# Optimization experiments

Measured on AMD Instinct MI355X. Metric: run time of the kernel, lower is better.

The kernel has to match this reference:

```python
import jax, jax.numpy as jnp
import numpy as np

B, S, DM = 2, 4096, 3584      # batch, seq_len, d_model (Zamba2-7B defaults)
H, DH = 112, 64               # n_heads, head_dim -> inner_dim = 7168
CHUNK = 256                   # chunk_size; S % CHUNK == 0 so no padding
INNER = H * DH


def setup_inputs() -> dict:
    key = jax.random.key(0)
    k1, k2, k3, k4 = jax.random.split(key, 4)
    return {
        "hidden_states": jax.random.normal(k1, (B, S, DM), jnp.float32),
        "W_in": jax.random.normal(k2, (2 * INNER, DM), jnp.float32) * 0.02,
        "W_out": jax.random.normal(k3, (DM, INNER), jnp.float32) * 0.02,
        "A_log": jax.random.normal(k4, (H,), jnp.float32),
    }


def reference(hidden_states, W_in, W_out, A_log):
    b, s, _ = hidden_states.shape
    # in_proj (nn.Linear, no bias): y = x @ W.T -> (b, s, 2*inner)
    xz = hidden_states @ W_in.T
    x, z = xz[..., :INNER], xz[..., INNER:]
    x = x.reshape(b, s, H, DH)

    n_chunks = s // CHUNK
    # (n_chunks, b, chunk, H, DH) for scan over chunks
    x_chunks = x.reshape(b, n_chunks, CHUNK, H, DH).transpose(1, 0, 2, 3, 4)

    A = jnp.exp(-jnp.abs(A_log)).astype(x.dtype).reshape(1, 1, H, 1)

    def step(h, xc):
        # per-position-within-chunk recurrence across chunks
        h = h * A + xc * 0.1
        return h, h

    h0 = jnp.zeros((b, CHUNK, H, DH), dtype=x.dtype)
    _, ys = jax.lax.scan(step, h0, x_chunks)  # (n_chunks, b, chunk, H, DH)

    y = ys.transpose(1, 0, 2, 3, 4).reshape(b, s, INNER)
    y = y * jax.nn.sigmoid(z)  # SiLU-style gate on z branch
    return y @ W_out.T
```

## Files before the change

### kernel.cpp

```cpp
#include <hip/hip_runtime.h>
#include <hip/hip_bf16.h>
#include <cstdint>
#include <cstddef>


typedef __bf16 bf16x8 __attribute__((ext_vector_type(8)));
typedef float f32x4 __attribute__((ext_vector_type(4)));
typedef unsigned short us8 __attribute__((ext_vector_type(8)));

__device__ __forceinline__ unsigned short f2bf(float f) {
  return __builtin_bit_cast(unsigned short, (__bf16)f);
}
__device__ __forceinline__ float bf2f(unsigned short u) {
  return (float)__builtin_bit_cast(__bf16, u);
}

__device__ __forceinline__ void async_lds16(const unsigned short* g, unsigned short* l) {
  __builtin_amdgcn_global_load_lds(
      (__attribute__((address_space(1))) void*)(size_t)(const void*)g,
      (__attribute__((address_space(3))) void*)l,
      16, 0, 0);
}

__global__ __launch_bounds__(256) void cvt_f32_bf16(
    const float* __restrict__ src, unsigned short* __restrict__ dst, int n4) {
  int t = blockIdx.x * 256 + threadIdx.x;
  if (t >= n4) return;
  float4 v = reinterpret_cast<const float4*>(src)[t];
  ushort4 o;
  o.x = f2bf(v.x); o.y = f2bf(v.y); o.z = f2bf(v.z); o.w = f2bf(v.w);
  reinterpret_cast<ushort4*>(dst)[t] = o;
}

template <bool OUT_BF16>
__global__ __launch_bounds__(256) void gemm_bt(
    const unsigned short* __restrict__ A, const unsigned short* __restrict__ Bm,
    void* __restrict__ Cv, int K, int lda, int ldb, int ldc) {
  __shared__ __align__(16) unsigned short As[128 * 64];
  __shared__ __align__(16) unsigned short Bs[128 * 64];

  const int lane = threadIdx.x & 63;
  const int wave = threadIdx.x >> 6;
  const int bm = blockIdx.y * 128;
  const int bn = blockIdx.x * 128;

  const int srow = lane >> 3;
  const int scol = ((lane & 7) ^ srow) * 8;
  const unsigned short* gA = A + (size_t)(bm + wave * 32 + srow) * lda + scol;
  const unsigned short* gB = Bm + (size_t)(bn + wave * 32 + srow) * ldb + scol;
  unsigned short* lA = As + wave * 2048;
  unsigned short* lB = Bs + wave * 2048;

  const int wm = wave & 1;
  const int wn = wave >> 1;
  const int l15 = lane & 15;
  const int kq = lane >> 4;
  const int s7 = l15 & 7;
  const int so0 = ((kq ^ s7) * 8);

  const unsigned short* fa = As + (wm * 64 + l15) * 64;
  const unsigned short* fb = Bs + (wn * 64 + l15) * 64;

  f32x4 acc[4][4];
#pragma unroll
  for (int i = 0; i < 4; ++i)
#pragma unroll
    for (int j = 0; j < 4; ++j) acc[i][j] = (f32x4){0.f, 0.f, 0.f, 0.f};

  for (int k0 = 0; k0 < K; k0 += 64) {
#pragma unroll
    for (int j = 0; j < 4; ++j) {
      async_lds16(gA + (size_t)(j * 8) * lda, lA + j * 512);
      async_lds16(gB + (size_t)(j * 8) * ldb, lB + j * 512);
    }
    __syncthreads();

#pragma unroll
    for (int sub = 0; sub < 2; ++sub) {
      const int so = so0 ^ (sub * 32);
      bf16x8 a[4], b[4];
#pragma unroll
      for (int i = 0; i < 4; ++i)
        a[i] = *reinterpret_cast<const bf16x8*>(fa + i * (16 * 64) + so);
#pragma unroll
      for (int j = 0; j < 4; ++j)
        b[j] = *reinterpret_cast<const bf16x8*>(fb + j * (16 * 64) + so);

#pragma unroll
      for (int i = 0; i < 4; ++i)
#pragma unroll
        for (int j = 0; j < 4; ++j)
          acc[i][j] = __builtin_amdgcn_mfma_f32_16x16x32_bf16(a[i], b[j], acc[i][j], 0, 0, 0);
    }

    gA += 64; gB += 64;
    __syncthreads();
  }

#pragma unroll
  for (int i = 0; i < 4; ++i) {
#pragma unroll
    for (int j = 0; j < 4; ++j) {
      const int col = bn + wn * 64 + j * 16 + l15;
#pragma unroll
      for (int r = 0; r < 4; ++r) {
        const int row = bm + wm * 64 + i * 16 + kq * 4 + r;
        if (OUT_BF16)
          ((unsigned short*)Cv)[(size_t)row * ldc + col] = f2bf(acc[i][j][r]);
        else
          ((float*)Cv)[(size_t)row * ldc + col] = acc[i][j][r];
      }
    }
  }
}

__global__ __launch_bounds__(256) void scan_gate(
    unsigned short* __restrict__ xz, const float* __restrict__ A_log) {
  const int tid = blockIdx.x * 256 + threadIdx.x;
  const int i8 = tid % 896;
  const int rb = tid / 896;
  const int r = rb & 255;
  const int b = rb >> 8;
  const int i = i8 * 8;
  const float Ah = __expf(-fabsf(A_log[i >> 6]));

  float st[8];
#pragma unroll
  for (int j = 0; j < 8; ++j) st[j] = 0.f;

  const size_t base = ((size_t)b * 4096 + r) * 14336 + i;
#pragma unroll
  for (int c = 0; c < 16; ++c) {
    const size_t off = base + (size_t)c * (256 * 14336);
    us8 xr = *reinterpret_cast<const us8*>(xz + off);
    us8 zr = *reinterpret_cast<const us8*>(xz + off + 7168);
    us8 yo;
#pragma unroll
    for (int j = 0; j < 8; ++j) {
      st[j] = st[j] * Ah + 0.1f * bf2f(xr[j]);
      const float zv = bf2f(zr[j]);
      const float sg = 1.f / (1.f + __expf(-zv));
      yo[j] = f2bf(st[j] * sg);
    }
    *reinterpret_cast<us8*>(xz + off) = yo;
  }
}

extern "C" void kernel_launch(void* const* d_in, const int* in_sizes, int n_in,
                              void* d_out, int out_size, void* d_ws, size_t ws_size,
                              hipStream_t stream) {
  const float* hidden = (const float*)d_in[0];
  const float* W_in   = (const float*)d_in[1];
  const float* W_out  = (const float*)d_in[2];
  const float* A_log  = (const float*)d_in[3];

  unsigned short* hid_bf  = (unsigned short*)d_ws;
  unsigned short* win_bf  = hid_bf  + 29360128ull;
  unsigned short* wout_bf = win_bf  + 51380224ull;
  unsigned short* xz      = wout_bf + 25690112ull;

  cvt_f32_bf16<<<29360128 / 4 / 256, 256, 0, stream>>>(hidden, hid_bf, 29360128 / 4);
  cvt_f32_bf16<<<51380224 / 4 / 256, 256, 0, stream>>>(W_in, win_bf, 51380224 / 4);
  cvt_f32_bf16<<<25690112 / 4 / 256, 256, 0, stream>>>(W_out, wout_bf, 25690112 / 4);

  gemm_bt<true><<<dim3(14336 / 128, 8192 / 128), 256, 0, stream>>>(
      hid_bf, win_bf, xz, 3584, 3584, 3584, 14336);

  scan_gate<<<1792, 256, 0, stream>>>(xz, A_log);

  gemm_bt<false><<<dim3(3584 / 128, 8192 / 128), 256, 0, stream>>>(
      xz, wout_bf, d_out, 7168, 14336, 7168, 3584);
}
```

Measured before the change: 1.940 ms.

## Replace 128x128 GEMM with double-buffered 256x256 tile, 8-wave pipelined kernel

Both GEMMs now use a 256x256 output tile computed by 512 threads. K-tiles are staged into a 128KB double-buffered LDS region with async global-to-LDS loads issued ahead of the MFMA phases, and waits use explicit vmcnt/lgkmcnt counters with barriers in place of full syncthreads. The change also adds a workgroup-index swizzle for L2 locality and s_setprio around the MFMA bursts. The aim is to overlap memory traffic with compute and raise data reuse per tile. In exchange it relies on hand-tuned wait counts, uses much more LDS per block, and launches fewer workgroups, which risks low occupancy and a tail effect on the smaller output GEMM.

```diff
diff --git a/kernel.cpp b/kernel.cpp
--- a/kernel.cpp
+++ b/kernel.cpp
@@ -33,82 +33,149 @@
 }
 
 template <bool OUT_BF16>
-__global__ __launch_bounds__(256) void gemm_bt(
+__global__ __launch_bounds__(512, 2) void gemm256(
     const unsigned short* __restrict__ A, const unsigned short* __restrict__ Bm,
     void* __restrict__ Cv, int K, int lda, int ldb, int ldc) {
-  __shared__ __align__(16) unsigned short As[128 * 64];
-  __shared__ __align__(16) unsigned short Bs[128 * 64];
-
-  const int lane = threadIdx.x & 63;
-  const int wave = threadIdx.x >> 6;
-  const int bm = blockIdx.y * 128;
-  const int bn = blockIdx.x * 128;
-
-  const int srow = lane >> 3;
-  const int scol = ((lane & 7) ^ srow) * 8;
-  const unsigned short* gA = A + (size_t)(bm + wave * 32 + srow) * lda + scol;
-  const unsigned short* gB = Bm + (size_t)(bn + wave * 32 + srow) * ldb + scol;
-  unsigned short* lA = As + wave * 2048;
-  unsigned short* lB = Bs + wave * 2048;
-
-  const int wm = wave & 1;
-  const int wn = wave >> 1;
+  __shared__ __align__(16) unsigned short lds[65536];
+
+  const int tid  = threadIdx.x;
+  const int lane = tid & 63;
+  const int wave = tid >> 6;
+
+  const int nbx  = gridDim.x;
+  const int nwg  = nbx * gridDim.y;
+  const int orig = blockIdx.y * nbx + blockIdx.x;
+  const int swz  = (orig & 7) * (nwg >> 3) + (orig >> 3);
+  const int bm   = (swz / nbx) * 256;
+  const int bn   = (swz % nbx) * 256;
+
+  const int wm  = wave >> 2;
+  const int wn  = wave & 3;
   const int l15 = lane & 15;
-  const int kq = lane >> 4;
-  const int s7 = l15 & 7;
-  const int so0 = ((kq ^ s7) * 8);
-
-  const unsigned short* fa = As + (wm * 64 + l15) * 64;
-  const unsigned short* fb = Bs + (wn * 64 + l15) * 64;
-
-  f32x4 acc[4][4];
-#pragma unroll
-  for (int i = 0; i < 4; ++i)
+  const int kq  = lane >> 4;
+  const int swzr = kq ^ ((l15 >> 1) & 3);
+  const int aoff = (wm * 128 + l15) * 32 + swzr * 8;
+  const int boff = (wn * 64  + l15) * 32 + swzr * 8;
+
+  const int srow = wave * 16 + (lane >> 2);
+  const int sg   = (lane & 3) ^ ((lane >> 3) & 3);
+  const unsigned short* gAr = A  + (size_t)(bm + srow) * lda + sg * 8;
+  const unsigned short* gBr = Bm + (size_t)(bn + srow) * ldb + sg * 8;
+
+  auto STAGE = [&](int t, int mat, int kh) {
+    unsigned short* ldst = lds + ((((t & 1) * 2 + mat) * 2 + kh) << 13) + wave * 512;
+    const unsigned short* g = (mat ? gBr : gAr) + t * 64 + kh * 32;
+    const size_t ldx = mat ? (size_t)ldb : (size_t)lda;
+    async_lds16(g, ldst);
+    async_lds16(g + 128 * ldx, ldst + 4096);
+  };
+
+  f32x4 acc[8][4];
+#pragma unroll
+  for (int i = 0; i < 8; ++i)
 #pragma unroll
     for (int j = 0; j < 4; ++j) acc[i][j] = (f32x4){0.f, 0.f, 0.f, 0.f};
 
-  for (int k0 = 0; k0 < K; k0 += 64) {
-#pragma unroll
-    for (int j = 0; j < 4; ++j) {
-      async_lds16(gA + (size_t)(j * 8) * lda, lA + j * 512);
-      async_lds16(gB + (size_t)(j * 8) * ldb, lB + j * 512);
-    }
-    __syncthreads();
-
-#pragma unroll
-    for (int sub = 0; sub < 2; ++sub) {
-      const int so = so0 ^ (sub * 32);
-      bf16x8 a[4], b[4];
-#pragma unroll
-      for (int i = 0; i < 4; ++i)
-        a[i] = *reinterpret_cast<const bf16x8*>(fa + i * (16 * 64) + so);
-#pragma unroll
-      for (int j = 0; j < 4; ++j)
-        b[j] = *reinterpret_cast<const bf16x8*>(fb + j * (16 * 64) + so);
-
-#pragma unroll
-      for (int i = 0; i < 4; ++i)
-#pragma unroll
-        for (int j = 0; j < 4; ++j)
-          acc[i][j] = __builtin_amdgcn_mfma_f32_16x16x32_bf16(a[i], b[j], acc[i][j], 0, 0, 0);
-    }
-
-    gA += 64; gB += 64;
-    __syncthreads();
-  }
-
-#pragma unroll
-  for (int i = 0; i < 4; ++i) {
+  const int NT = K >> 6;
+
+  STAGE(0, 0, 0); STAGE(0, 1, 0); STAGE(0, 0, 1); STAGE(0, 1, 1);
+  if (NT > 1) {
+    STAGE(1, 1, 0); STAGE(1, 0, 0); STAGE(1, 1, 1);
+    asm volatile("s_waitcnt vmcnt(6)" ::: "memory");
+  } else {
+    asm volatile("s_waitcnt vmcnt(0)" ::: "memory");
+  }
+  __builtin_amdgcn_s_barrier();
+
+  for (int t = 0; t < NT; ++t) {
+    const unsigned short* Ak0 = lds + (t & 1) * 32768;
+    const unsigned short* Ak1 = Ak0 + 8192;
+    const unsigned short* Bk0 = Ak0 + 16384;
+    const unsigned short* Bk1 = Ak0 + 24576;
+
+    bf16x8 a[4], b[4];
+
+#pragma unroll
+    for (int i = 0; i < 4; ++i)
+      a[i] = *reinterpret_cast<const bf16x8*>(Ak0 + aoff + i * 512);
+#pragma unroll
+    for (int j = 0; j < 4; ++j)
+      b[j] = *reinterpret_cast<const bf16x8*>(Bk0 + boff + j * 512);
+    if (t + 1 < NT) STAGE(t + 1, 0, 1);
+    __builtin_amdgcn_s_barrier();
+    asm volatile("s_waitcnt lgkmcnt(0)" ::: "memory");
+    __builtin_amdgcn_s_setprio(1);
+#pragma unroll
+    for (int i = 0; i < 4; ++i)
+#pragma unroll
+      for (int j = 0; j < 4; ++j)
+        acc[i][j] = __builtin_amdgcn_mfma_f32_16x16x32_bf16(a[i], b[j], acc[i][j], 0, 0, 0);
+    __builtin_amdgcn_s_setprio(0);
+    __builtin_amdgcn_s_barrier();
+
+#pragma unroll
+    for (int i = 0; i < 4; ++i)
+      a[i] = *reinterpret_cast<const bf16x8*>(Ak0 + aoff + 2048 + i * 512);
+    if (t + 2 < NT) STAGE(t + 2, 1, 0);
+    __builtin_amdgcn_s_barrier();
+    asm volatile("s_waitcnt lgkmcnt(0)" ::: "memory");
+    __builtin_amdgcn_s_setprio(1);
+#pragma unroll
+    for (int i = 0; i < 4; ++i)
+#pragma unroll
+      for (int j = 0; j < 4; ++j)
+        acc[4 + i][j] = __builtin_amdgcn_mfma_f32_16x16x32_bf16(a[i], b[j], acc[4 + i][j], 0, 0, 0);
+    __builtin_amdgcn_s_setprio(0);
+    __builtin_amdgcn_s_barrier();
+
+#pragma unroll
+    for (int i = 0; i < 4; ++i)
+      a[i] = *reinterpret_cast<const bf16x8*>(Ak1 + aoff + i * 512);
+#pragma unroll
+    for (int j = 0; j < 4; ++j)
+      b[j] = *reinterpret_cast<const bf16x8*>(Bk1 + boff + j * 512);
+    if (t + 2 < NT) STAGE(t + 2, 0, 0);
+    __builtin_amdgcn_s_barrier();
+    asm volatile("s_waitcnt lgkmcnt(0)" ::: "memory");
+    __builtin_amdgcn_s_setprio(1);
+#pragma unroll
+    for (int i = 0; i < 4; ++i)
+#pragma unroll
+      for (int j = 0; j < 4; ++j)
+        acc[i][j] = __builtin_amdgcn_mfma_f32_16x16x32_bf16(a[i], b[j], acc[i][j], 0, 0, 0);
+    __builtin_amdgcn_s_setprio(0);
+    __builtin_amdgcn_s_barrier();
+
+#pragma unroll
+    for (int i = 0; i < 4; ++i)
+      a[i] = *reinterpret_cast<const bf16x8*>(Ak1 + aoff + 2048 + i * 512);
+    if (t + 2 < NT) STAGE(t + 2, 1, 1);
+    __builtin_amdgcn_s_barrier();
+    asm volatile("s_waitcnt lgkmcnt(0)" ::: "memory");
+    __builtin_amdgcn_s_setprio(1);
+#pragma unroll
+    for (int i = 0; i < 4; ++i)
+#pragma unroll
+      for (int j = 0; j < 4; ++j)
+        acc[4 + i][j] = __builtin_amdgcn_mfma_f32_16x16x32_bf16(a[i], b[j], acc[4 + i][j], 0, 0, 0);
+    __builtin_amdgcn_s_setprio(0);
+    if (t == NT - 2)      asm volatile("s_waitcnt vmcnt(0)" ::: "memory");
+    else if (t < NT - 2)  asm volatile("s_waitcnt vmcnt(6)" ::: "memory");
+    __builtin_amdgcn_s_barrier();
+  }
+
+#pragma unroll
+  for (int mi = 0; mi < 8; ++mi) {
 #pragma unroll
     for (int j = 0; j < 4; ++j) {
       const int col = bn + wn * 64 + j * 16 + l15;
 #pragma unroll
       for (int r = 0; r < 4; ++r) {
-        const int row = bm + wm * 64 + i * 16 + kq * 4 + r;
+        const int row = bm + wm * 128 + mi * 16 + kq * 4 + r;
         if (OUT_BF16)
-          ((unsigned short*)Cv)[(size_t)row * ldc + col] = f2bf(acc[i][j][r]);
+          ((unsigned short*)Cv)[(size_t)row * ldc + col] = f2bf(acc[mi][j][r]);
         else
-          ((float*)Cv)[(size_t)row * ldc + col] = acc[i][j][r];
+          ((float*)Cv)[(size_t)row * ldc + col] = acc[mi][j][r];
       }
     }
   }
@@ -163,11 +230,11 @@
   cvt_f32_bf16<<<51380224 / 4 / 256, 256, 0, stream>>>(W_in, win_bf, 51380224 / 4);
   cvt_f32_bf16<<<25690112 / 4 / 256, 256, 0, stream>>>(W_out, wout_bf, 25690112 / 4);
 
-  gemm_bt<true><<<dim3(14336 / 128, 8192 / 128), 256, 0, stream>>>(
+  gemm256<true><<<dim3(14336 / 256, 8192 / 256), 512, 0, stream>>>(
       hid_bf, win_bf, xz, 3584, 3584, 3584, 14336);
 
   scan_gate<<<1792, 256, 0, stream>>>(xz, A_log);
 
-  gemm_bt<false><<<dim3(3584 / 128, 8192 / 128), 256, 0, stream>>>(
+  gemm256<false><<<dim3(3584 / 256, 8192 / 256), 512, 0, stream>>>(
       xz, wout_bf, d_out, 7168, 14336, 7168, 3584);
 }
```

After: 1.648 ms. 15.1% less time.
